# Kernel optimization log

Measured on AMD Instinct MI355X. Metric: run time of the kernel, lower is better.

Reference implementation:

```python
import jax, jax.numpy as jnp
import numpy as np

N = 6144      # number of pedestrians
HID = 256     # hidden_dim
OUT = 32      # out_dim
NTOP = 4      # n nearest neighbours
EMB = OUT // NTOP  # per-neighbour embedding dim = 8


def setup_inputs() -> dict:
    key = jax.random.key(0)
    ks = jax.random.split(key, 12)
    r = lambda k, shp, s=1.0: (jax.random.normal(k, shp, dtype=jnp.float32) * s)
    return {
        "obs1": r(ks[0], (N, 2)),
        "obs2": r(ks[1], (N, 2)),
        "h": r(ks[2], (N, HID), 0.1),
        "c": r(ks[3], (N, HID), 0.1),
        "W_emb": r(ks[4], (4, EMB), 0.3),
        "b_emb": r(ks[5], (EMB,), 0.1),
        "W_ih": r(ks[6], (4 * HID, OUT), 0.1),
        "b_ih": r(ks[7], (4 * HID,), 0.1),
        "W_hh": r(ks[8], (4 * HID, HID), 0.1),
        "b_hh": r(ks[9], (4 * HID,), 0.1),
        "W_pool": r(ks[10], (OUT, HID), 0.1),
        "b_pool": r(ks[11], (OUT,), 0.1),
    }


def reference(obs1, obs2, h, c, W_emb, b_emb, W_ih, b_ih, W_hh, b_hh, W_pool, b_pool):
    n = obs2.shape[0]
    vel = obs2 - obs1                                   # [N,2]
    # rel_position[i, j] = obs2[j] - obs2[i]
    diff = obs2[None, :, :] - obs2[:, None, :]          # [N,N,2]
    dist = jnp.linalg.norm(diff, axis=-1)               # [N,N]
    # exclude self (torch code drops the diagonal before topk)
    dist = jnp.where(jnp.eye(n, dtype=bool), jnp.inf, dist)
    _, idx = jax.lax.top_k(-dist, NTOP)                 # [N,NTOP] indices of nearest
    nearest_pos = jnp.take_along_axis(diff, idx[:, :, None], axis=1)  # [N,NTOP,2]
    # rel_direction[i, j] = vel[j] - vel[i]
    nearest_vel = vel[idx] - vel[:, None, :]            # [N,NTOP,2]
    feat = jnp.concatenate([nearest_pos, nearest_vel], axis=-1)       # [N,NTOP,4]
    # Linear(4, EMB) + ReLU, then flatten neighbours -> [N, OUT]
    emb = jax.nn.relu(feat @ W_emb + b_emb).reshape(n, -1)
    # LSTMCell (PyTorch gate order: i, f, g, o)
    gates = emb @ W_ih.T + b_ih + h @ W_hh.T + b_hh     # [N,4*HID]
    gi, gf, gg, go = jnp.split(gates, 4, axis=-1)
    c_new = jax.nn.sigmoid(gf) * c + jax.nn.sigmoid(gi) * jnp.tanh(gg)
    h_new = jax.nn.sigmoid(go) * jnp.tanh(c_new)
    out = h_new @ W_pool.T + b_pool                     # [N,OUT]
    return out
```

## Files before the change

### kernel.cpp

```cpp
#include <hip/hip_runtime.h>
#include <math.h>

typedef unsigned short u16;
typedef unsigned long long u64;
typedef _Float16 f16;
typedef __attribute__((ext_vector_type(8))) short bf16x8;
typedef __attribute__((ext_vector_type(4))) float f32x4;

__device__ __forceinline__ float sigf(float x)  { return 1.0f / (1.0f + __expf(-x)); }
__device__ __forceinline__ float tanhf_(float x){ float e = __expf(2.0f * x); return 1.0f - 2.0f / (e + 1.0f); }
__device__ __forceinline__ u16 f2bf(float f) {
    unsigned x = __float_as_uint(f);
    return (u16)((x + 0x7fffu + ((x >> 16) & 1u)) >> 16);
}

#define INSU(KEY) do {                                                              \
    u64 _k = (KEY);                                                                 \
    k3 = (_k < k3) ? _k : k3;                                                       \
    { bool _c = k3 < k2; u64 _lo = _c ? k3 : k2, _hi = _c ? k2 : k3; k2 = _lo; k3 = _hi; } \
    { bool _c = k2 < k1; u64 _lo = _c ? k2 : k1, _hi = _c ? k1 : k2; k1 = _lo; k2 = _hi; } \
    { bool _c = k1 < k0; u64 _lo = _c ? k1 : k0, _hi = _c ? k0 : k1; k0 = _lo; k1 = _hi; } \
} while (0)

#define INS4(D, J) do {                                                              \
    float _d = (D); int _j = (J);                                                    \
    if (_d < bd3 || (_d == bd3 && _j < bj3)) {                                       \
        bd3 = _d; bj3 = _j;                                                          \
        if (bd3 < bd2 || (bd3 == bd2 && bj3 < bj2)) {                                \
            float _t = bd2; bd2 = bd3; bd3 = _t; int _u = bj2; bj2 = bj3; bj3 = _u; }\
        if (bd2 < bd1 || (bd2 == bd1 && bj2 < bj1)) {                                \
            float _t = bd1; bd1 = bd2; bd2 = _t; int _u = bj1; bj1 = bj2; bj2 = _u; }\
        if (bd1 < bd0 || (bd1 == bd0 && bj1 < bj0)) {                                \
            float _t = bd0; bd0 = bd1; bd1 = _t; int _u = bj0; bj0 = bj1; bj1 = _u; }\
    } } while (0)

__global__ void diag_kernel(float* out, int code, int out_size) {
    if (out_size > 0) out[0] = (float)code * 1.0e8f;
}

__global__ __launch_bounds__(256) void knn_prep_kernel(
    const float* __restrict__ obs1, const float* __restrict__ obs2,
    const float* __restrict__ Wemb, const float* __restrict__ bemb,
    const float* __restrict__ Wih,  const float* __restrict__ Whh,
    const float* __restrict__ Wp,
    u16* __restrict__ Wgf, u16* __restrict__ Wpf,
    int n, int knn_blocks, float* __restrict__ out)
{
    const int t = threadIdx.x;

    if (blockIdx.x >= knn_blocks) {
        int id = (blockIdx.x - knn_blocks) * 256 + t;
        if (id < 36864) {
            int gt = id / 576, rem = id - gt * 576;
            int kt = rem >> 6, ln = rem & 63;
            int g  = gt * 16 + (ln & 15);
            int k  = kt * 32 + (ln >> 4) * 8;
            u16* dst = Wgf + (size_t)id * 8;
            #pragma unroll
            for (int j = 0; j < 8; j++) {
                int kk = k + j;
                float v = (kk < 32) ? Wih[(size_t)g * 32 + kk]
                                    : Whh[(size_t)g * 256 + (kk - 32)];
                dst[j] = f2bf(v);
            }
        } else if (id < 37888) {
            int id2 = id - 36864;
            int pt = id2 >> 9, rem = id2 & 511;
            int kt = rem >> 6, ln = rem & 63;
            int o  = pt * 16 + (ln & 15);
            int k  = kt * 32 + (ln >> 4) * 8;
            u16* dst = Wpf + (size_t)id2 * 8;
            #pragma unroll
            for (int j = 0; j < 8; j++)
                dst[j] = f2bf(Wp[(size_t)o * 256 + k + j]);
        }
        return;
    }

    const int lane = t & 63;
    const int wv   = t >> 6;
    const int i    = blockIdx.x * 4 + wv;
    if (i >= n) return;

    const float2* o2 = (const float2*)obs2;
    const float2 pi = o2[i];

    u64 k0 = ~0ull, k1 = ~0ull, k2 = ~0ull, k3 = ~0ull;

    int j = lane;
    for (; j + 192 < n; j += 256) {
        float2 p0 = o2[j], p1 = o2[j + 64], p2 = o2[j + 128], p3 = o2[j + 192];
        float dx, dy, d2, dd; u64 key;
        dx = p0.x - pi.x; dy = p0.y - pi.y;
        d2 = __fadd_rn(__fmul_rn(dx, dx), __fmul_rn(dy, dy));
        dd = __fsqrt_rn(d2);
        key = (((u64)__float_as_uint(dd)) << 24) | (unsigned)j;
        key = (j == i) ? ~0ull : key;                         INSU(key);
        dx = p1.x - pi.x; dy = p1.y - pi.y;
        d2 = __fadd_rn(__fmul_rn(dx, dx), __fmul_rn(dy, dy));
        dd = __fsqrt_rn(d2);
        key = (((u64)__float_as_uint(dd)) << 24) | (unsigned)(j + 64);
        key = (j + 64 == i) ? ~0ull : key;                    INSU(key);
        dx = p2.x - pi.x; dy = p2.y - pi.y;
        d2 = __fadd_rn(__fmul_rn(dx, dx), __fmul_rn(dy, dy));
        dd = __fsqrt_rn(d2);
        key = (((u64)__float_as_uint(dd)) << 24) | (unsigned)(j + 128);
        key = (j + 128 == i) ? ~0ull : key;                   INSU(key);
        dx = p3.x - pi.x; dy = p3.y - pi.y;
        d2 = __fadd_rn(__fmul_rn(dx, dx), __fmul_rn(dy, dy));
        dd = __fsqrt_rn(d2);
        key = (((u64)__float_as_uint(dd)) << 24) | (unsigned)(j + 192);
        key = (j + 192 == i) ? ~0ull : key;                   INSU(key);
    }
    for (; j < n; j += 64) {
        float2 pj = o2[j];
        float dx = pj.x - pi.x, dy = pj.y - pi.y;
        float d2 = __fadd_rn(__fmul_rn(dx, dx), __fmul_rn(dy, dy));
        float dd = __fsqrt_rn(d2);
        u64 key = (((u64)__float_as_uint(dd)) << 24) | (unsigned)j;
        key = (j == i) ? ~0ull : key;
        INSU(key);
    }

    #pragma unroll
    for (int m = 1; m < 64; m <<= 1) {
        u64 o0 = __shfl_xor(k0, m), o1 = __shfl_xor(k1, m);
        u64 o2_ = __shfl_xor(k2, m), o3 = __shfl_xor(k3, m);
        INSU(o0); INSU(o1); INSU(o2_); INSU(o3);
    }

    if (lane < 4) {
        u64 kq = (lane == 0) ? k0 : (lane == 1) ? k1 : (lane == 2) ? k2 : k3;
        int jn = (int)(kq & 0xFFFFFF);
        if (jn < 0 || jn >= n) jn = 0;
        float pix = pi.x, piy = pi.y;
        float pjx = obs2[2 * jn], pjy = obs2[2 * jn + 1];
        float px = pjx - pix, py = pjy - piy;
        float vix = pix - obs1[2 * i];
        float viy = piy - obs1[2 * i + 1];
        float vx = (pjx - obs1[2 * jn])     - vix;
        float vy = (pjy - obs1[2 * jn + 1]) - viy;
        float* dst = out + (size_t)i * 32 + lane * 8;
        #pragma unroll
        for (int e = 0; e < 8; e++) {
            float a = px * Wemb[e]      + py * Wemb[8 + e]
                    + vx * Wemb[16 + e] + vy * Wemb[24 + e]
                    + bemb[e];
            dst[e] = fmaxf(a, 0.0f);
        }
    }
}

__global__ __launch_bounds__(256) void lstm_kernel(
    const float* __restrict__ h,   const float* __restrict__ c,
    const u16*  __restrict__ Wgf,  const float* __restrict__ bih,
    const float* __restrict__ bhh,
    const u16*  __restrict__ Wpf,  const float* __restrict__ bp,
    int n, float* __restrict__ out)
{
    __shared__ __align__(16) char lds[42816];
    u16* sXb  = (u16*)lds;
    f16* gbuf = (f16*)(lds + 9472);
    u16* sHb  = (u16*)lds;

    const int t    = threadIdx.x;
    const int i0   = blockIdx.x * 16;
    const int lane = t & 63;
    const int wv   = t >> 6;
    const int fm   = lane & 15;
    const int fq   = lane >> 4;

    if (t < 128) {
        int r = t >> 3, k4 = (t & 7) * 4;
        int row = i0 + r;
        float4 ev = (row < n) ? ((const float4*)out)[(size_t)row * 8 + (k4 >> 2)]
                              : make_float4(0.f, 0.f, 0.f, 0.f);
        u16* d = &sXb[r * 296 + k4];
        d[0] = f2bf(ev.x); d[1] = f2bf(ev.y); d[2] = f2bf(ev.z); d[3] = f2bf(ev.w);
    }
    for (int f = t; f < 16 * 64; f += 256) {
        int r = f >> 6, k4 = f & 63;
        int row = i0 + r;
        float4 hv = (row < n) ? ((const float4*)h)[(size_t)row * 64 + k4]
                              : make_float4(0.f, 0.f, 0.f, 0.f);
        u16* d = &sXb[r * 296 + 32 + k4 * 4];
        d[0] = f2bf(hv.x); d[1] = f2bf(hv.y); d[2] = f2bf(hv.z); d[3] = f2bf(hv.w);
    }
    __syncthreads();

    bf16x8 afr[9];
    #pragma unroll
    for (int kt = 0; kt < 9; kt++)
        afr[kt] = *(const bf16x8*)&sXb[fm * 296 + kt * 32 + fq * 8];

    #pragma unroll 2
    for (int nt = 0; nt < 16; nt++) {
        const int gt = wv * 16 + nt;
        const u16* wbase = Wgf + ((size_t)gt * 9) * 512 + lane * 8;
        f32x4 acc = {0.f, 0.f, 0.f, 0.f};
        #pragma unroll
        for (int kt = 0; kt < 9; kt++) {
            bf16x8 bfr = *(const bf16x8*)(wbase + kt * 512);
            acc = __builtin_amdgcn_mfma_f32_16x16x32_bf16(afr[kt], bfr, acc, 0, 0, 0);
        }
        #pragma unroll
        for (int r_ = 0; r_ < 4; r_++)
            gbuf[(fq * 4 + r_) * 1042 + gt * 16 + fm] = (f16)acc[r_];
    }
    __syncthreads();

    {
        const int u = t;
        float b0 = bih[u]       + bhh[u];
        float b1 = bih[u + 256] + bhh[u + 256];
        float b2 = bih[u + 512] + bhh[u + 512];
        float b3 = bih[u + 768] + bhh[u + 768];
        for (int r = 0; r < 16; r++) {
            int row = i0 + r;
            float cin = (row < n) ? c[(size_t)row * 256 + u] : 0.0f;
            float gi = (float)gbuf[r * 1042 + u]       + b0;
            float gf = (float)gbuf[r * 1042 + u + 256] + b1;
            float gg = (float)gbuf[r * 1042 + u + 512] + b2;
            float go = (float)gbuf[r * 1042 + u + 768] + b3;
            float cn = sigf(gf) * cin + sigf(gi) * tanhf_(gg);
            float hn = sigf(go) * tanhf_(cn);
            sHb[r * 264 + u] = f2bf(hn);
        }
    }
    __syncthreads();

    if (wv < 2) {
        bf16x8 ah[8];
        #pragma unroll
        for (int kt = 0; kt < 8; kt++)
            ah[kt] = *(const bf16x8*)&sHb[fm * 264 + kt * 32 + fq * 8];
        const u16* wbase = Wpf + ((size_t)wv * 8) * 512 + lane * 8;
        f32x4 acc = {0.f, 0.f, 0.f, 0.f};
        #pragma unroll
        for (int kt = 0; kt < 8; kt++) {
            bf16x8 bfr = *(const bf16x8*)(wbase + kt * 512);
            acc = __builtin_amdgcn_mfma_f32_16x16x32_bf16(ah[kt], bfr, acc, 0, 0, 0);
        }
        float bias = bp[wv * 16 + fm];
        #pragma unroll
        for (int r_ = 0; r_ < 4; r_++) {
            int row = i0 + fq * 4 + r_;
            if (row < n) out[(size_t)row * 32 + wv * 16 + fm] = acc[r_] + bias;
        }
    }
}

__global__ __launch_bounds__(256) void nnlstm_fallback(
    const float* __restrict__ obs1, const float* __restrict__ obs2,
    const float* __restrict__ h,    const float* __restrict__ c,
    const float* __restrict__ Wemb, const float* __restrict__ bemb,
    const float* __restrict__ Wih,  const float* __restrict__ bih,
    const float* __restrict__ Whh,  const float* __restrict__ bhh,
    const float* __restrict__ Wp,   const float* __restrict__ bp,
    int n, float* __restrict__ out)
{
    __shared__ float sMd[16][64];
    __shared__ int   sMj[16][64];
    __shared__ float sX[16][292];
    __shared__ float sH[16][264];

    const int t   = threadIdx.x;
    const int sub = t & 15;
    const int ii  = t >> 4;
    const int i0  = blockIdx.x * 16;
    const int i   = i0 + ii;

    for (int v = t; v < 16 * 256; v += 256) {
        int r = v >> 8, k = v & 255;
        int row = i0 + r;
        sX[r][32 + k] = (row < n) ? h[(size_t)row * 256 + k] : 0.0f;
    }

    float bd0 = 1e30f, bd1 = 1e30f, bd2 = 1e30f, bd3 = 1e30f;
    int   bj0 = 0x7fffffff, bj1 = 0x7fffffff, bj2 = 0x7fffffff, bj3 = 0x7fffffff;

    if (i < n) {
        const float pix = obs2[2 * i];
        const float piy = obs2[2 * i + 1];
        for (int j = sub; j < n; j += 16) {
            float dx = obs2[2 * j]     - pix;
            float dy = obs2[2 * j + 1] - piy;
            float d2 = __fadd_rn(__fmul_rn(dx, dx), __fmul_rn(dy, dy));
            float dist = __fsqrt_rn(d2);
            if (j == i) continue;
            INS4(dist, j);
        }
    }
    sMd[ii][sub * 4 + 0] = bd0;  sMj[ii][sub * 4 + 0] = bj0;
    sMd[ii][sub * 4 + 1] = bd1;  sMj[ii][sub * 4 + 1] = bj1;
    sMd[ii][sub * 4 + 2] = bd2;  sMj[ii][sub * 4 + 2] = bj2;
    sMd[ii][sub * 4 + 3] = bd3;  sMj[ii][sub * 4 + 3] = bj3;
    __syncthreads();

    if (t < 16) {
        const int r = t;
        const int irow = i0 + r;
        float bd0 = 1e30f, bd1 = 1e30f, bd2 = 1e30f, bd3 = 1e30f;
        int   bj0 = 0x7fffffff, bj1 = 0x7fffffff, bj2 = 0x7fffffff, bj3 = 0x7fffffff;
        for (int q = 0; q < 64; q++) { INS4(sMd[r][q], sMj[r][q]); }

        if (irow < n) {
            float pix = obs2[2 * irow], piy = obs2[2 * irow + 1];
            float vix = pix - obs1[2 * irow];
            float viy = piy - obs1[2 * irow + 1];
            #pragma unroll
            for (int q2 = 0; q2 < 4; q2++) {
                int jn = (q2 == 0) ? bj0 : (q2 == 1) ? bj1 : (q2 == 2) ? bj2 : bj3;
                if (jn < 0 || jn >= n) jn = 0;
                float pjx = obs2[2 * jn], pjy = obs2[2 * jn + 1];
                float px = pjx - pix, py = pjy - piy;
                float vx = (pjx - obs1[2 * jn])     - vix;
                float vy = (pjy - obs1[2 * jn + 1]) - viy;
                #pragma unroll
                for (int e = 0; e < 8; e++) {
                    float a = px * Wemb[e]      + py * Wemb[8 + e]
                            + vx * Wemb[16 + e] + vy * Wemb[24 + e]
                            + bemb[e];
                    sX[r][q2 * 8 + e] = fmaxf(a, 0.0f);
                }
            }
        } else {
            for (int e = 0; e < 32; e++) sX[r][e] = 0.0f;
        }
    }
    __syncthreads();

    const int uu = t;
    float acc[4][16];
    #pragma unroll
    for (int j = 0; j < 4; j++) {
        float b = bih[uu + 256 * j] + bhh[uu + 256 * j];
        #pragma unroll
        for (int r = 0; r < 16; r++) acc[j][r] = b;
    }

    for (int kc = 0; kc < 288; kc++) {
        float w[4];
        #pragma unroll
        for (int j = 0; j < 4; j++) {
            int g = uu + 256 * j;
            w[j] = (kc < 32) ? Wih[(size_t)g * 32 + kc]
                             : Whh[(size_t)g * 256 + (kc - 32)];
        }
        #pragma unroll
        for (int r = 0; r < 16; r++) {
            float x = sX[r][kc];
            #pragma unroll
            for (int j = 0; j < 4; j++) acc[j][r] += w[j] * x;
        }
    }

    for (int r = 0; r < 16; r++) {
        int row = i0 + r;
        float cin = (row < n) ? c[(size_t)row * 256 + uu] : 0.0f;
        float cn = sigf(acc[1][r]) * cin + sigf(acc[0][r]) * tanhf(acc[2][r]);
        float hn = sigf(acc[3][r]) * tanhf(cn);
        sH[r][uu] = hn;
    }
    __syncthreads();

    for (int v = t; v < 16 * 32; v += 256) {
        int r = v >> 5, o = v & 31;
        int row = i0 + r;
        if (row >= n) continue;
        float a = bp[o];
        for (int kc = 0; kc < 256; kc++)
            a += Wp[(size_t)o * 256 + kc] * sH[r][kc];
        out[(size_t)row * 32 + o] = a;
    }
}

extern "C" void kernel_launch(void* const* d_in, const int* in_sizes, int n_in,
                              void* d_out, int out_size, void* d_ws, size_t ws_size,
                              hipStream_t stream) {
    float* out = (float*)d_out;

    int code = 0, n = 0;
    if (n_in != 12) code = 1;
    else {
        n = in_sizes[1] / 2;
        if (n <= 4 || in_sizes[1] != 2 * n)          code = 2;
        else if (in_sizes[0]  != 2 * n)              code = 3;
        else if (in_sizes[2]  != 256 * n)            code = 4;
        else if (in_sizes[3]  != 256 * n)            code = 5;
        else if (in_sizes[4]  != 32 || in_sizes[5] != 8)        code = 6;
        else if (in_sizes[6]  != 32768 || in_sizes[7] != 1024)  code = 7;
        else if (in_sizes[8]  != 262144 || in_sizes[9] != 1024) code = 8;
        else if (in_sizes[10] != 8192 || in_sizes[11] != 32)    code = 9;
        else if (out_size != 32 * n)                 code = 10;
    }
    if (code != 0) {
        diag_kernel<<<1, 1, 0, stream>>>(out, code, out_size);
        return;
    }

    const float* obs1   = (const float*)d_in[0];
    const float* obs2   = (const float*)d_in[1];
    const float* h      = (const float*)d_in[2];
    const float* c      = (const float*)d_in[3];
    const float* W_emb  = (const float*)d_in[4];
    const float* b_emb  = (const float*)d_in[5];
    const float* W_ih   = (const float*)d_in[6];
    const float* b_ih   = (const float*)d_in[7];
    const float* W_hh   = (const float*)d_in[8];
    const float* b_hh   = (const float*)d_in[9];
    const float* W_pool = (const float*)d_in[10];
    const float* b_pool = (const float*)d_in[11];

    const size_t wgf_bytes = (size_t)36864 * 8 * sizeof(u16);
    const size_t wpf_bytes = (size_t)1024 * 8 * sizeof(u16);

    if (ws_size >= wgf_bytes + wpf_bytes && n <= (1 << 24)) {
        u16* Wgf = (u16*)d_ws;
        u16* Wpf = (u16*)((char*)d_ws + wgf_bytes);
        int knn_blocks = (n + 3) / 4;
        knn_prep_kernel<<<knn_blocks + 148, 256, 0, stream>>>(
            obs1, obs2, W_emb, b_emb, W_ih, W_hh, W_pool, Wgf, Wpf,
            n, knn_blocks, out);
        lstm_kernel<<<(n + 15) / 16, 256, 0, stream>>>(
            h, c, Wgf, b_ih, b_hh, Wpf, b_pool, n, out);
    } else {
        nnlstm_fallback<<<(n + 15) / 16, 256, 0, stream>>>(
            obs1, obs2, h, c, W_emb, b_emb, W_ih, b_ih, W_hh, b_hh,
            W_pool, b_pool, n, out);
    }
}
```

Before: 159.0 us.

## Fuse LSTM gate epilogue into MFMA registers, drop f16 gate buffer

The LSTM kernel now computes all four gate tiles (i,f,g,o) for the same hidden unit in one wave, so the sigmoid/tanh cell update runs straight from MFMA accumulator registers. This removes the large f16 LDS gate buffer, one barrier, and the f16 rounding of gate values. The block grows to 512 threads with 8 waves, each handling two unit tiles. LDS use drops sharply, but each thread holds more accumulators and the register pressure may limit occupancy.

```diff
diff --git a/kernel.cpp b/kernel.cpp
--- a/kernel.cpp
+++ b/kernel.cpp
@@ -3,7 +3,6 @@
 
 typedef unsigned short u16;
 typedef unsigned long long u64;
-typedef _Float16 f16;
 typedef __attribute__((ext_vector_type(8))) short bf16x8;
 typedef __attribute__((ext_vector_type(4))) float f32x4;
 
@@ -151,17 +150,16 @@
     }
 }
 
-__global__ __launch_bounds__(256) void lstm_kernel(
+__global__ __launch_bounds__(512) void lstm_kernel(
     const float* __restrict__ h,   const float* __restrict__ c,
     const u16*  __restrict__ Wgf,  const float* __restrict__ bih,
     const float* __restrict__ bhh,
     const u16*  __restrict__ Wpf,  const float* __restrict__ bp,
     int n, float* __restrict__ out)
 {
-    __shared__ __align__(16) char lds[42816];
-    u16* sXb  = (u16*)lds;
-    f16* gbuf = (f16*)(lds + 9472);
-    u16* sHb  = (u16*)lds;
+    __shared__ __align__(16) char lds[17920];
+    u16* sXb = (u16*)lds;
+    u16* sHb = (u16*)(lds + 9472);
 
     const int t    = threadIdx.x;
     const int i0   = blockIdx.x * 16;
@@ -170,15 +168,14 @@
     const int fm   = lane & 15;
     const int fq   = lane >> 4;
 
-    if (t < 128) {
-        int r = t >> 3, k4 = (t & 7) * 4;
+    {
+        int r = t >> 5, e = t & 31;
         int row = i0 + r;
-        float4 ev = (row < n) ? ((const float4*)out)[(size_t)row * 8 + (k4 >> 2)]
-                              : make_float4(0.f, 0.f, 0.f, 0.f);
-        u16* d = &sXb[r * 296 + k4];
-        d[0] = f2bf(ev.x); d[1] = f2bf(ev.y); d[2] = f2bf(ev.z); d[3] = f2bf(ev.w);
-    }
-    for (int f = t; f < 16 * 64; f += 256) {
+        float v = (row < n) ? out[(size_t)row * 32 + e] : 0.0f;
+        sXb[r * 296 + e] = f2bf(v);
+    }
+    #pragma unroll
+    for (int f = t; f < 16 * 64; f += 512) {
         int r = f >> 6, k4 = f & 63;
         int row = i0 + r;
         float4 hv = (row < n) ? ((const float4*)h)[(size_t)row * 64 + k4]
@@ -193,38 +190,42 @@
     for (int kt = 0; kt < 9; kt++)
         afr[kt] = *(const bf16x8*)&sXb[fm * 296 + kt * 32 + fq * 8];
 
-    #pragma unroll 2
-    for (int nt = 0; nt < 16; nt++) {
-        const int gt = wv * 16 + nt;
-        const u16* wbase = Wgf + ((size_t)gt * 9) * 512 + lane * 8;
-        f32x4 acc = {0.f, 0.f, 0.f, 0.f};
-        #pragma unroll
-        for (int kt = 0; kt < 9; kt++) {
-            bf16x8 bfr = *(const bf16x8*)(wbase + kt * 512);
-            acc = __builtin_amdgcn_mfma_f32_16x16x32_bf16(afr[kt], bfr, acc, 0, 0, 0);
-        }
-        #pragma unroll
-        for (int r_ = 0; r_ < 4; r_++)
-            gbuf[(fq * 4 + r_) * 1042 + gt * 16 + fm] = (f16)acc[r_];
-    }
-    __syncthreads();
-
-    {
-        const int u = t;
+    #pragma unroll
+    for (int ut2 = 0; ut2 < 2; ut2++) {
+        const int ut = wv * 2 + ut2;
+        const int u  = ut * 16 + fm;
+
+        f32x4 acc[4];
+        #pragma unroll
+        for (int jg = 0; jg < 4; jg++) acc[jg] = (f32x4){0.f, 0.f, 0.f, 0.f};
+
+        #pragma unroll
+        for (int jg = 0; jg < 4; jg++) {
+            const int gt = jg * 16 + ut;
+            const u16* wbase = Wgf + ((size_t)gt * 9) * 512 + lane * 8;
+            #pragma unroll
+            for (int kt = 0; kt < 9; kt++) {
+                bf16x8 bfr = *(const bf16x8*)(wbase + kt * 512);
+                acc[jg] = __builtin_amdgcn_mfma_f32_16x16x32_bf16(afr[kt], bfr, acc[jg], 0, 0, 0);
+            }
+        }
+
         float b0 = bih[u]       + bhh[u];
         float b1 = bih[u + 256] + bhh[u + 256];
         float b2 = bih[u + 512] + bhh[u + 512];
         float b3 = bih[u + 768] + bhh[u + 768];
-        for (int r = 0; r < 16; r++) {
-            int row = i0 + r;
+
+        #pragma unroll
+        for (int r_ = 0; r_ < 4; r_++) {
+            int row = i0 + fq * 4 + r_;
             float cin = (row < n) ? c[(size_t)row * 256 + u] : 0.0f;
-            float gi = (float)gbuf[r * 1042 + u]       + b0;
-            float gf = (float)gbuf[r * 1042 + u + 256] + b1;
-            float gg = (float)gbuf[r * 1042 + u + 512] + b2;
-            float go = (float)gbuf[r * 1042 + u + 768] + b3;
+            float gi = acc[0][r_] + b0;
+            float gf = acc[1][r_] + b1;
+            float gg = acc[2][r_] + b2;
+            float go = acc[3][r_] + b3;
             float cn = sigf(gf) * cin + sigf(gi) * tanhf_(gg);
             float hn = sigf(go) * tanhf_(cn);
-            sHb[r * 264 + u] = f2bf(hn);
+            sHb[(fq * 4 + r_) * 264 + u] = f2bf(hn);
         }
     }
     __syncthreads();
@@ -422,7 +423,7 @@
         knn_prep_kernel<<<knn_blocks + 148, 256, 0, stream>>>(
             obs1, obs2, W_emb, b_emb, W_ih, W_hh, W_pool, Wgf, Wpf,
             n, knn_blocks, out);
-        lstm_kernel<<<(n + 15) / 16, 256, 0, stream>>>(
+        lstm_kernel<<<(n + 15) / 16, 512, 0, stream>>>(
             h, c, Wgf, b_ih, b_hh, Wpf, b_pool, n, out);
     } else {
         nnlstm_fallback<<<(n + 15) / 16, 256, 0, stream>>>(
```

Measured after the change: 153.1 us. 3.7% less time.
